# Performance work log

Measured on AMD Instinct MI355X. Metric: run time of the kernel, lower is better.

## Reference

```python
import jax, jax.numpy as jnp
import numpy as np

N, J, P = 512, 20000, 8   # samples, genes (rna_count), covariates
DIM = J - 1               # pivot=True drops one column from the softmax logits


def setup_inputs() -> dict:
    key = jax.random.key(0)
    k0, k1, k2, k3, k4 = jax.random.split(key, 5)
    X = jax.random.normal(k0, (N, P), dtype=jnp.float32)
    # counts: non-negative integers stored as float (matches torch float64 Y of counts)
    Y = jnp.round(jax.random.uniform(k1, (N, J), dtype=jnp.float32) * 1000.0)
    mu = jax.random.normal(k2, (DIM,), dtype=jnp.float32)
    beta = jax.random.normal(k3, (P * DIM,), dtype=jnp.float32) * 0.1
    phi = jax.random.normal(k4, (J,), dtype=jnp.float32)
    return {"mu": mu, "beta": beta, "phi": phi, "X": X, "Y": Y}


def _nb_loglik(y, mean, disp):
    # NB with mean `mean` and dispersion `disp` (var = mean + disp*mean^2):
    # r = 1/disp, p = r/(r+mean)
    # log pmf = lgamma(y+r) - lgamma(r) - lgamma(y+1) + r*log(p) + y*log(1-p)
    r = 1.0 / disp
    log_rpm = jnp.log(r + mean)
    return (jax.lax.lgamma(y + r) - jax.lax.lgamma(r) - jax.lax.lgamma(y + 1.0)
            + r * (jnp.log(r) - log_rpm)
            + y * (jnp.log(mean) - log_rpm))


def reference(mu, beta, phi, X, Y):
    n, p = X.shape
    dim = mu.shape[0]
    beta_ = beta.reshape(p, dim)
    logits = mu + X @ beta_                                   # [N, J-1]
    logits = jnp.concatenate(
        [logits, jnp.zeros((n, 1), dtype=logits.dtype)], axis=1)  # pivot column of zeros -> [N, J]
    pi = jax.nn.softmax(logits, axis=1)                       # exp(logits - logsumexp)
    s = jnp.sum(Y, axis=1, keepdims=True)                     # [N, 1] total counts per sample
    mean = s * pi                                             # [N, J]
    disp = jax.nn.softplus(phi)                               # [J]
    log_lik = jnp.sum(_nb_loglik(Y, mean, disp))
    return log_lik.reshape(1)
```

## Files before the change

### kernel.cpp

```cpp
#include <hip/hip_runtime.h>

constexpr int N_SAMPLES = 512;
constexpr int J_GENES   = 20000;
constexpr int P_COV     = 8;
constexpr int DIM       = J_GENES - 1;
constexpr int BLOCK     = 256;
constexpr int TABLE_N   = 1024;

constexpr int CHUNK_G   = 1024;
constexpr int G_CHUNKS  = (J_GENES + CHUNK_G - 1) / CHUNK_G;
constexpr int ROWS      = 8;
constexpr int RGROUPS   = N_SAMPLES / ROWS;

constexpr size_t WS_RW    = 0;
constexpr size_t WS_K     = WS_RW    + J_GENES;
constexpr size_t WS_MUP   = WS_K     + J_GENES;
constexpr size_t WS_BETAP = WS_MUP   + J_GENES;
constexpr size_t WS_LGYT  = WS_BETAP + (size_t)P_COV * J_GENES;
constexpr size_t WS_SACC  = WS_LGYT  + TABLE_N;
constexpr size_t WS_EACC  = WS_SACC  + N_SAMPLES;
constexpr size_t WS_TOTAL = WS_EACC  + N_SAMPLES;

__device__ inline float wave_reduce_sum(float v) {
#pragma unroll
    for (int off = 32; off > 0; off >>= 1)
        v += __shfl_down(v, off, 64);
    return v;
}

__device__ inline float lgamma_pos(float z) {
    float corr = 0.0f;
    if (z < 2.0f) {
        corr = -__logf(z * (z + 1.0f));
        z += 2.0f;
    }
    float lz  = __logf(z);
    float rz  = __builtin_amdgcn_rcpf(z);
    float rz2 = rz * rz;
    float ser = rz * fmaf(rz2, fmaf(rz2, 7.9365079365e-4f, -2.7777777778e-3f),
                          8.3333333333e-2f);
    return fmaf(z - 0.5f, lz, 0.91893853320467274f - z + ser + corr);
}

__global__ __launch_bounds__(BLOCK) void prep_kernel(
    const float* __restrict__ mu, const float* __restrict__ beta,
    const float* __restrict__ phi, float* __restrict__ ws,
    float* __restrict__ out) {
    int j = blockIdx.x * blockDim.x + threadIdx.x;
    if (j == 0) out[0] = 0.0f;
    if (j < N_SAMPLES) { ws[WS_SACC + j] = 0.0f; ws[WS_EACC + j] = 0.0f; }
    if (j < TABLE_N)   ws[WS_LGYT + j] = lgammaf((float)j + 1.0f);
    if (j < J_GENES) {
        float ph = phi[j];
        float sp = (ph > 20.0f) ? ph : log1pf(__expf(ph));
        float r  = 1.0f / sp;
        float lr = -__logf(sp);
        ws[WS_RW  + j] = r;
        ws[WS_K   + j] = fmaf(r, lr, -lgammaf(r));
        ws[WS_MUP + j] = (j < DIM) ? mu[j] : 0.0f;
#pragma unroll
        for (int p = 0; p < P_COV; ++p)
            ws[WS_BETAP + (size_t)p * J_GENES + j] =
                (j < DIM) ? beta[p * DIM + j] : 0.0f;
    }
}

__global__ __launch_bounds__(BLOCK, 4) void sums_kernel(
    const float* __restrict__ X, const float* __restrict__ Y,
    const float* __restrict__ ws_c, float* __restrict__ ws) {
    const int t  = threadIdx.x;
    const int j0 = blockIdx.x * CHUNK_G + t * 4;
    const bool valid = j0 < J_GENES;

    float4 mu4 = make_float4(0.f, 0.f, 0.f, 0.f);
    float4 bp[P_COV];
#pragma unroll
    for (int p = 0; p < P_COV; ++p) bp[p] = make_float4(0.f, 0.f, 0.f, 0.f);
    if (valid) {
        mu4 = *(const float4*)(ws_c + WS_MUP + j0);
#pragma unroll
        for (int p = 0; p < P_COV; ++p)
            bp[p] = *(const float4*)(ws_c + WS_BETAP + (size_t)p * J_GENES + j0);
    }

    __shared__ float redS[BLOCK / 64], redE[BLOCK / 64];

    for (int rr = 0; rr < ROWS; ++rr) {
        const int n = blockIdx.y * ROWS + rr;
        float x[P_COV];
#pragma unroll
        for (int p = 0; p < P_COV; ++p) x[p] = X[n * P_COV + p];

        float sa = 0.0f, ea = 0.0f;
        if (valid) {
            float4 y4 = *(const float4*)(Y + (size_t)n * J_GENES + j0);
            float4 lg = mu4;
#pragma unroll
            for (int p = 0; p < P_COV; ++p) {
                lg.x = fmaf(x[p], bp[p].x, lg.x);
                lg.y = fmaf(x[p], bp[p].y, lg.y);
                lg.z = fmaf(x[p], bp[p].z, lg.z);
                lg.w = fmaf(x[p], bp[p].w, lg.w);
            }
            sa = (y4.x + y4.y) + (y4.z + y4.w);
            ea = (__expf(lg.x) + __expf(lg.y)) + (__expf(lg.z) + __expf(lg.w));
        }
        float vs = wave_reduce_sum(sa);
        float ve = wave_reduce_sum(ea);
        if ((t & 63) == 0) { redS[t >> 6] = vs; redE[t >> 6] = ve; }
        __syncthreads();
        if (t == 0) {
            atomicAdd(&ws[WS_SACC + n], (redS[0] + redS[1]) + (redS[2] + redS[3]));
            atomicAdd(&ws[WS_EACC + n], (redE[0] + redE[1]) + (redE[2] + redE[3]));
        }
        __syncthreads();
    }
}

__device__ inline float nb_elem(float y, float lg, float r, float K,
                                float c, float logc,
                                const float* __restrict__ tbl) {
    float el   = __expf(lg);
    float mean = c * el;
    float z    = y + r;
    float lrm  = __logf(r + mean);
    float lgyr = lgamma_pos(z);
    float lgy1 = tbl[(int)(y + 0.5f)];
    return (lgyr - lgy1 + K) + fmaf(-z, lrm, y * (logc + lg));
}

__global__ __launch_bounds__(BLOCK, 4) void nb_kernel(
    const float* __restrict__ X, const float* __restrict__ Y,
    const float* __restrict__ ws_c, float* __restrict__ out) {
    const int t  = threadIdx.x;
    const int j0 = blockIdx.x * CHUNK_G + t * 4;
    const bool valid = j0 < J_GENES;

    __shared__ __align__(16) float tbl[TABLE_N];
    *(float4*)&tbl[t * 4] = *(const float4*)(ws_c + WS_LGYT + t * 4);

    float4 mu4 = make_float4(0.f, 0.f, 0.f, 0.f);
    float4 r4  = make_float4(1.f, 1.f, 1.f, 1.f);
    float4 K4  = make_float4(0.f, 0.f, 0.f, 0.f);
    float4 bp[P_COV];
#pragma unroll
    for (int p = 0; p < P_COV; ++p) bp[p] = make_float4(0.f, 0.f, 0.f, 0.f);
    if (valid) {
        mu4 = *(const float4*)(ws_c + WS_MUP + j0);
        r4  = *(const float4*)(ws_c + WS_RW  + j0);
        K4  = *(const float4*)(ws_c + WS_K   + j0);
#pragma unroll
        for (int p = 0; p < P_COV; ++p)
            bp[p] = *(const float4*)(ws_c + WS_BETAP + (size_t)p * J_GENES + j0);
    }
    __syncthreads();

    float acc = 0.0f;
    for (int rr = 0; rr < ROWS; ++rr) {
        const int n = blockIdx.y * ROWS + rr;
        const float s = ws_c[WS_SACC + n];
        const float E = ws_c[WS_EACC + n];
        const float c = s / E;
        const float logc = __logf(c);

        float x[P_COV];
#pragma unroll
        for (int p = 0; p < P_COV; ++p) x[p] = X[n * P_COV + p];

        if (valid) {
            float4 y4 = *(const float4*)(Y + (size_t)n * J_GENES + j0);
            float4 lg = mu4;
#pragma unroll
            for (int p = 0; p < P_COV; ++p) {
                lg.x = fmaf(x[p], bp[p].x, lg.x);
                lg.y = fmaf(x[p], bp[p].y, lg.y);
                lg.z = fmaf(x[p], bp[p].z, lg.z);
                lg.w = fmaf(x[p], bp[p].w, lg.w);
            }
            acc += nb_elem(y4.x, lg.x, r4.x, K4.x, c, logc, tbl);
            acc += nb_elem(y4.y, lg.y, r4.y, K4.y, c, logc, tbl);
            acc += nb_elem(y4.z, lg.z, r4.z, K4.z, c, logc, tbl);
            acc += nb_elem(y4.w, lg.w, r4.w, K4.w, c, logc, tbl);
        }
    }

    float v = wave_reduce_sum(acc);
    __shared__ float red[BLOCK / 64];
    if ((t & 63) == 0) red[t >> 6] = v;
    __syncthreads();
    if (t == 0)
        atomicAdd(out, (red[0] + red[1]) + (red[2] + red[3]));
}

__global__ __launch_bounds__(BLOCK) void nb_mono(
    const float* __restrict__ mu, const float* __restrict__ beta,
    const float* __restrict__ phi, const float* __restrict__ X,
    const float* __restrict__ Y, float* __restrict__ out) {
    const int n = blockIdx.x;
    const int t = threadIdx.x;
    __shared__ float red[4];
    __shared__ float sh_s, sh_lse, sh_logs;
    float x[P_COV];
#pragma unroll
    for (int p = 0; p < P_COV; ++p) x[p] = X[n * P_COV + p];
    const float* yrow = Y + (size_t)n * J_GENES;
    float s_acc = 0.0f, e_acc = 0.0f;
    for (int j = t; j < J_GENES; j += BLOCK) {
        float logit = 0.0f;
        if (j < DIM) {
            logit = mu[j];
#pragma unroll
            for (int p = 0; p < P_COV; ++p)
                logit = fmaf(x[p], beta[p * DIM + j], logit);
        }
        s_acc += yrow[j];
        e_acc += __expf(logit);
    }
    float v = wave_reduce_sum(s_acc);
    if ((t & 63) == 0) red[t >> 6] = v;
    __syncthreads();
    if (t == 0) { float st = red[0]+red[1]+red[2]+red[3]; sh_s = st; sh_logs = __logf(st); }
    __syncthreads();
    v = wave_reduce_sum(e_acc);
    if ((t & 63) == 0) red[t >> 6] = v;
    __syncthreads();
    if (t == 0) sh_lse = __logf(red[0]+red[1]+red[2]+red[3]);
    __syncthreads();
    const float s = sh_s, logs = sh_logs, lse = sh_lse;
    float acc = 0.0f;
    for (int j = t; j < J_GENES; j += BLOCK) {
        float logit = 0.0f;
        if (j < DIM) {
            logit = mu[j];
#pragma unroll
            for (int p = 0; p < P_COV; ++p)
                logit = fmaf(x[p], beta[p * DIM + j], logit);
        }
        float ph = phi[j];
        float sp = (ph > 20.0f) ? ph : log1pf(__expf(ph));
        float r  = 1.0f / sp;
        float y  = yrow[j];
        float lp = logit - lse;
        float mean = s * __expf(lp);
        float lrm  = __logf(r + mean);
        acc += lgamma_pos(y + r) - lgamma_pos(r) - lgamma_pos(y + 1.0f)
             + fmaf(r, -__logf(sp) - lrm, y * ((logs + lp) - lrm));
    }
    v = wave_reduce_sum(acc);
    if ((t & 63) == 0) red[t >> 6] = v;
    __syncthreads();
    if (t == 0) atomicAdd(out, (red[0]+red[1])+(red[2]+red[3]));
}

__global__ void zero_out_kernel(float* __restrict__ out) { out[0] = 0.0f; }

extern "C" void kernel_launch(void* const* d_in, const int* in_sizes, int n_in,
                              void* d_out, int out_size, void* d_ws, size_t ws_size,
                              hipStream_t stream) {
    const float* mu   = (const float*)d_in[0];
    const float* beta = (const float*)d_in[1];
    const float* phi  = (const float*)d_in[2];
    const float* X    = (const float*)d_in[3];
    const float* Y    = (const float*)d_in[4];
    float* out = (float*)d_out;
    float* ws  = (float*)d_ws;

    if (ws_size >= WS_TOTAL * sizeof(float)) {
        dim3 grid(G_CHUNKS, RGROUPS);
        prep_kernel<<<(J_GENES + BLOCK - 1) / BLOCK, BLOCK, 0, stream>>>(
            mu, beta, phi, ws, out);
        sums_kernel<<<grid, BLOCK, 0, stream>>>(X, Y, ws, ws);
        nb_kernel<<<grid, BLOCK, 0, stream>>>(X, Y, ws, out);
    } else {
        zero_out_kernel<<<1, 1, 0, stream>>>(out);
        nb_mono<<<N_SAMPLES, BLOCK, 0, stream>>>(mu, beta, phi, X, Y, out);
    }
}
```

Baseline: 123.6 us.

## Fuse prep into row-sum kernel and replace atomics with per-chunk partials

```diff
diff --git a/kernel.cpp b/kernel.cpp
--- a/kernel.cpp
+++ b/kernel.cpp
@@ -13,13 +13,10 @@
 constexpr int RGROUPS   = N_SAMPLES / ROWS;
 
 constexpr size_t WS_RW    = 0;
-constexpr size_t WS_K     = WS_RW    + J_GENES;
-constexpr size_t WS_MUP   = WS_K     + J_GENES;
-constexpr size_t WS_BETAP = WS_MUP   + J_GENES;
-constexpr size_t WS_LGYT  = WS_BETAP + (size_t)P_COV * J_GENES;
-constexpr size_t WS_SACC  = WS_LGYT  + TABLE_N;
-constexpr size_t WS_EACC  = WS_SACC  + N_SAMPLES;
-constexpr size_t WS_TOTAL = WS_EACC  + N_SAMPLES;
+constexpr size_t WS_KW    = WS_RW + J_GENES;
+constexpr size_t WS_PS    = WS_KW + J_GENES;
+constexpr size_t WS_PE    = WS_PS + (size_t)N_SAMPLES * G_CHUNKS;
+constexpr size_t WS_TOTAL = WS_PE + (size_t)N_SAMPLES * G_CHUNKS;
 
 __device__ inline float wave_reduce_sum(float v) {
 #pragma unroll
@@ -42,51 +39,55 @@
     return fmaf(z - 0.5f, lz, 0.91893853320467274f - z + ser + corr);
 }
 
-__global__ __launch_bounds__(BLOCK) void prep_kernel(
+__device__ inline void load_gene_consts(const float* __restrict__ mu,
+                                        const float* __restrict__ beta,
+                                        int j0, bool valid,
+                                        float muv[4], float bv[P_COV][4]) {
+#pragma unroll
+    for (int i = 0; i < 4; ++i) {
+        const int j = j0 + i;
+        const bool in = valid && (j < DIM);
+        muv[i] = in ? mu[j] : 0.0f;
+#pragma unroll
+        for (int p = 0; p < P_COV; ++p)
+            bv[p][i] = in ? beta[p * DIM + j] : 0.0f;
+    }
+}
+
+__global__ __launch_bounds__(BLOCK) void phaseA_kernel(
     const float* __restrict__ mu, const float* __restrict__ beta,
-    const float* __restrict__ phi, float* __restrict__ ws,
+    const float* __restrict__ phi, const float* __restrict__ X,
+    const float* __restrict__ Y, float* __restrict__ ws,
     float* __restrict__ out) {
-    int j = blockIdx.x * blockDim.x + threadIdx.x;
-    if (j == 0) out[0] = 0.0f;
-    if (j < N_SAMPLES) { ws[WS_SACC + j] = 0.0f; ws[WS_EACC + j] = 0.0f; }
-    if (j < TABLE_N)   ws[WS_LGYT + j] = lgammaf((float)j + 1.0f);
-    if (j < J_GENES) {
-        float ph = phi[j];
-        float sp = (ph > 20.0f) ? ph : log1pf(__expf(ph));
-        float r  = 1.0f / sp;
-        float lr = -__logf(sp);
-        ws[WS_RW  + j] = r;
-        ws[WS_K   + j] = fmaf(r, lr, -lgammaf(r));
-        ws[WS_MUP + j] = (j < DIM) ? mu[j] : 0.0f;
-#pragma unroll
-        for (int p = 0; p < P_COV; ++p)
-            ws[WS_BETAP + (size_t)p * J_GENES + j] =
-                (j < DIM) ? beta[p * DIM + j] : 0.0f;
-    }
-}
-
-__global__ __launch_bounds__(BLOCK, 4) void sums_kernel(
-    const float* __restrict__ X, const float* __restrict__ Y,
-    const float* __restrict__ ws_c, float* __restrict__ ws) {
     const int t  = threadIdx.x;
-    const int j0 = blockIdx.x * CHUNK_G + t * 4;
+    const int bx = blockIdx.x, by = blockIdx.y;
+    const int j0 = bx * CHUNK_G + t * 4;
     const bool valid = j0 < J_GENES;
 
-    float4 mu4 = make_float4(0.f, 0.f, 0.f, 0.f);
-    float4 bp[P_COV];
-#pragma unroll
-    for (int p = 0; p < P_COV; ++p) bp[p] = make_float4(0.f, 0.f, 0.f, 0.f);
-    if (valid) {
-        mu4 = *(const float4*)(ws_c + WS_MUP + j0);
-#pragma unroll
-        for (int p = 0; p < P_COV; ++p)
-            bp[p] = *(const float4*)(ws_c + WS_BETAP + (size_t)p * J_GENES + j0);
-    }
-
-    __shared__ float redS[BLOCK / 64], redE[BLOCK / 64];
+    if (by == 0) {
+        if (bx == 0 && t == 0) out[0] = 0.0f;
+        if (valid) {
+#pragma unroll
+            for (int i = 0; i < 4; ++i) {
+                const int j = j0 + i;
+                float ph = phi[j];
+                float sp = (ph > 20.0f) ? ph : log1pf(__expf(ph));
+                float r  = 1.0f / sp;
+                float lr = -__logf(sp);
+                ws[WS_RW + j] = r;
+                ws[WS_KW + j] = fmaf(r, lr, -lgamma_pos(r));
+            }
+        }
+    }
+
+    float muv[4], bv[P_COV][4];
+    load_gene_consts(mu, beta, j0, valid, muv, bv);
+
+    __shared__ float redS[2][4], redE[2][4];
+    const int n0 = by * ROWS;
 
     for (int rr = 0; rr < ROWS; ++rr) {
-        const int n = blockIdx.y * ROWS + rr;
+        const int n = n0 + rr;
         float x[P_COV];
 #pragma unroll
         for (int p = 0; p < P_COV; ++p) x[p] = X[n * P_COV + p];
@@ -94,98 +95,115 @@
         float sa = 0.0f, ea = 0.0f;
         if (valid) {
             float4 y4 = *(const float4*)(Y + (size_t)n * J_GENES + j0);
-            float4 lg = mu4;
-#pragma unroll
-            for (int p = 0; p < P_COV; ++p) {
-                lg.x = fmaf(x[p], bp[p].x, lg.x);
-                lg.y = fmaf(x[p], bp[p].y, lg.y);
-                lg.z = fmaf(x[p], bp[p].z, lg.z);
-                lg.w = fmaf(x[p], bp[p].w, lg.w);
+            float lg[4];
+#pragma unroll
+            for (int i = 0; i < 4; ++i) {
+                float v = muv[i];
+#pragma unroll
+                for (int p = 0; p < P_COV; ++p) v = fmaf(x[p], bv[p][i], v);
+                lg[i] = v;
             }
             sa = (y4.x + y4.y) + (y4.z + y4.w);
-            ea = (__expf(lg.x) + __expf(lg.y)) + (__expf(lg.z) + __expf(lg.w));
-        }
+            ea = (__expf(lg[0]) + __expf(lg[1])) + (__expf(lg[2]) + __expf(lg[3]));
+        }
+
         float vs = wave_reduce_sum(sa);
         float ve = wave_reduce_sum(ea);
-        if ((t & 63) == 0) { redS[t >> 6] = vs; redE[t >> 6] = ve; }
+        const int b = rr & 1;
+        if ((t & 63) == 0) { redS[b][t >> 6] = vs; redE[b][t >> 6] = ve; }
         __syncthreads();
         if (t == 0) {
-            atomicAdd(&ws[WS_SACC + n], (redS[0] + redS[1]) + (redS[2] + redS[3]));
-            atomicAdd(&ws[WS_EACC + n], (redE[0] + redE[1]) + (redE[2] + redE[3]));
-        }
-        __syncthreads();
+            ws[WS_PS + (size_t)n * G_CHUNKS + bx] =
+                (redS[b][0] + redS[b][1]) + (redS[b][2] + redS[b][3]);
+            ws[WS_PE + (size_t)n * G_CHUNKS + bx] =
+                (redE[b][0] + redE[b][1]) + (redE[b][2] + redE[b][3]);
+        }
     }
 }
 
 __device__ inline float nb_elem(float y, float lg, float r, float K,
                                 float c, float logc,
                                 const float* __restrict__ tbl) {
-    float el   = __expf(lg);
-    float mean = c * el;
+    float mean = c * __expf(lg);
     float z    = y + r;
     float lrm  = __logf(r + mean);
-    float lgyr = lgamma_pos(z);
-    float lgy1 = tbl[(int)(y + 0.5f)];
-    return (lgyr - lgy1 + K) + fmaf(-z, lrm, y * (logc + lg));
-}
-
-__global__ __launch_bounds__(BLOCK, 4) void nb_kernel(
+    int   yi   = (int)(y + 0.5f);
+    float lgy1 = (yi < TABLE_N) ? tbl[yi] : lgamma_pos(y + 1.0f);
+    return (lgamma_pos(z) - lgy1 + K) + fmaf(-z, lrm, y * (logc + lg));
+}
+
+__global__ __launch_bounds__(BLOCK) void phaseB_kernel(
+    const float* __restrict__ mu, const float* __restrict__ beta,
     const float* __restrict__ X, const float* __restrict__ Y,
     const float* __restrict__ ws_c, float* __restrict__ out) {
     const int t  = threadIdx.x;
-    const int j0 = blockIdx.x * CHUNK_G + t * 4;
+    const int bx = blockIdx.x, by = blockIdx.y;
+    const int j0 = bx * CHUNK_G + t * 4;
     const bool valid = j0 < J_GENES;
+    const int n0 = by * ROWS;
 
     __shared__ __align__(16) float tbl[TABLE_N];
-    *(float4*)&tbl[t * 4] = *(const float4*)(ws_c + WS_LGYT + t * 4);
-
-    float4 mu4 = make_float4(0.f, 0.f, 0.f, 0.f);
-    float4 r4  = make_float4(1.f, 1.f, 1.f, 1.f);
-    float4 K4  = make_float4(0.f, 0.f, 0.f, 0.f);
-    float4 bp[P_COV];
-#pragma unroll
-    for (int p = 0; p < P_COV; ++p) bp[p] = make_float4(0.f, 0.f, 0.f, 0.f);
+    __shared__ float shS[ROWS], shE[ROWS], shc[ROWS], shlc[ROWS];
+
+#pragma unroll
+    for (int i = 0; i < 4; ++i) {
+        const int k = t * 4 + i;
+        tbl[k] = (k < 2) ? 0.0f : lgamma_pos((float)k + 1.0f);
+    }
+    if (t < 2 * ROWS) {
+        const int r = t & (ROWS - 1);
+        const int which = t >> 3;
+        const float* src = ws_c + (which ? WS_PE : WS_PS)
+                         + (size_t)(n0 + r) * G_CHUNKS;
+        float a = 0.0f;
+#pragma unroll
+        for (int k = 0; k < G_CHUNKS; ++k) a += src[k];
+        if (which) shE[r] = a; else shS[r] = a;
+    }
+    __syncthreads();
+    if (t < ROWS) {
+        float c = shS[t] / shE[t];
+        shc[t]  = c;
+        shlc[t] = __logf(c);
+    }
+
+    float muv[4], bv[P_COV][4];
+    load_gene_consts(mu, beta, j0, valid, muv, bv);
+    float4 r4 = make_float4(1.f, 1.f, 1.f, 1.f);
+    float4 K4 = make_float4(0.f, 0.f, 0.f, 0.f);
     if (valid) {
-        mu4 = *(const float4*)(ws_c + WS_MUP + j0);
-        r4  = *(const float4*)(ws_c + WS_RW  + j0);
-        K4  = *(const float4*)(ws_c + WS_K   + j0);
-#pragma unroll
-        for (int p = 0; p < P_COV; ++p)
-            bp[p] = *(const float4*)(ws_c + WS_BETAP + (size_t)p * J_GENES + j0);
+        r4 = *(const float4*)(ws_c + WS_RW + j0);
+        K4 = *(const float4*)(ws_c + WS_KW + j0);
     }
     __syncthreads();
 
     float acc = 0.0f;
     for (int rr = 0; rr < ROWS; ++rr) {
-        const int n = blockIdx.y * ROWS + rr;
-        const float s = ws_c[WS_SACC + n];
-        const float E = ws_c[WS_EACC + n];
-        const float c = s / E;
-        const float logc = __logf(c);
-
+        const int n = n0 + rr;
+        const float c = shc[rr], logc = shlc[rr];
         float x[P_COV];
 #pragma unroll
         for (int p = 0; p < P_COV; ++p) x[p] = X[n * P_COV + p];
 
         if (valid) {
             float4 y4 = *(const float4*)(Y + (size_t)n * J_GENES + j0);
-            float4 lg = mu4;
-#pragma unroll
-            for (int p = 0; p < P_COV; ++p) {
-                lg.x = fmaf(x[p], bp[p].x, lg.x);
-                lg.y = fmaf(x[p], bp[p].y, lg.y);
-                lg.z = fmaf(x[p], bp[p].z, lg.z);
-                lg.w = fmaf(x[p], bp[p].w, lg.w);
+            float lg[4];
+#pragma unroll
+            for (int i = 0; i < 4; ++i) {
+                float v = muv[i];
+#pragma unroll
+                for (int p = 0; p < P_COV; ++p) v = fmaf(x[p], bv[p][i], v);
+                lg[i] = v;
             }
-            acc += nb_elem(y4.x, lg.x, r4.x, K4.x, c, logc, tbl);
-            acc += nb_elem(y4.y, lg.y, r4.y, K4.y, c, logc, tbl);
-            acc += nb_elem(y4.z, lg.z, r4.z, K4.z, c, logc, tbl);
-            acc += nb_elem(y4.w, lg.w, r4.w, K4.w, c, logc, tbl);
+            acc += nb_elem(y4.x, lg[0], r4.x, K4.x, c, logc, tbl);
+            acc += nb_elem(y4.y, lg[1], r4.y, K4.y, c, logc, tbl);
+            acc += nb_elem(y4.z, lg[2], r4.z, K4.z, c, logc, tbl);
+            acc += nb_elem(y4.w, lg[3], r4.w, K4.w, c, logc, tbl);
         }
     }
 
     float v = wave_reduce_sum(acc);
-    __shared__ float red[BLOCK / 64];
+    __shared__ float red[4];
     if ((t & 63) == 0) red[t >> 6] = v;
     __syncthreads();
     if (t == 0)
@@ -267,10 +285,8 @@
 
     if (ws_size >= WS_TOTAL * sizeof(float)) {
         dim3 grid(G_CHUNKS, RGROUPS);
-        prep_kernel<<<(J_GENES + BLOCK - 1) / BLOCK, BLOCK, 0, stream>>>(
-            mu, beta, phi, ws, out);
-        sums_kernel<<<grid, BLOCK, 0, stream>>>(X, Y, ws, ws);
-        nb_kernel<<<grid, BLOCK, 0, stream>>>(X, Y, ws, out);
+        phaseA_kernel<<<grid, BLOCK, 0, stream>>>(mu, beta, phi, X, Y, ws, out);
+        phaseB_kernel<<<grid, BLOCK, 0, stream>>>(mu, beta, X, Y, ws, out);
     } else {
         zero_out_kernel<<<1, 1, 0, stream>>>(out);
         nb_mono<<<N_SAMPLES, BLOCK, 0, stream>>>(mu, beta, phi, X, Y, out);
```

After: 127.5 us. 3.2% more time.
